# Optimization experiments

Hardware: AMD Instinct MI355X
Metric: run time of the kernel (lower is better)

The kernel has to match this reference:

```python
import jax, jax.numpy as jnp
import numpy as np

B, S, D = 64, 2048, 512

def setup_inputs() -> dict:
    key = jax.random.key(0)
    k1, k2, k3, k4, k5 = jax.random.split(key, 5)
    x = jax.random.normal(k1, (B, S, D), dtype=jnp.float32)
    # torch Linear(dim, dim): weight [D, D], bias [D]
    W1 = jax.random.normal(k2, (D, D), dtype=jnp.float32) * (1.0 / np.sqrt(D))
    b1 = jax.random.normal(k3, (D,), dtype=jnp.float32) * 0.01
    # torch Linear(dim, 1): weight [1, D] -> stored as [D], bias scalar
    w2 = jax.random.normal(k4, (D,), dtype=jnp.float32) * (1.0 / np.sqrt(D))
    b2 = jax.random.normal(k5, (), dtype=jnp.float32) * 0.01
    return {"x": x, "W1": W1, "b1": b1, "w2": w2, "b2": b2}

def reference(x, W1, b1, w2, b2):
    # score MLP: Linear -> Tanh -> Linear(->1), squeeze
    h = jnp.tanh(jnp.einsum('bsd,ed->bse', x, W1) + b1)   # [B,S,D]
    scores = jnp.einsum('bsd,d->bs', h, w2) + b2          # [B,S]
    w = jax.nn.softmax(scores, axis=1)[..., None]         # [B,S,1]
    ctx = jnp.sum(x * w, axis=1)                          # [B,D]
    return (ctx, w)
```

## Files before the change

### kernel.cpp

```cpp
#include <hip/hip_runtime.h>
#include <hip/hip_bf16.h>

#define BB 64
#define SS 2048
#define DD 512
#define MTOT (BB * SS)

typedef __attribute__((ext_vector_type(8))) short short8;
typedef __attribute__((ext_vector_type(4))) short s16x4;
typedef __attribute__((ext_vector_type(4))) float f32x4;

__device__ __forceinline__ short f2bf(float f){
  __hip_bfloat16 h = __float2bfloat16(f);
  return *reinterpret_cast<short*>(&h);
}
__device__ __forceinline__ short8 pack8(float4 a, float4 b){
  short8 u;
  u[0]=f2bf(a.x); u[1]=f2bf(a.y); u[2]=f2bf(a.z); u[3]=f2bf(a.w);
  u[4]=f2bf(b.x); u[5]=f2bf(b.y); u[6]=f2bf(b.z); u[7]=f2bf(b.w);
  return u;
}
__device__ __forceinline__ s16x4 pack4(float4 a){
  s16x4 u;
  u[0]=f2bf(a.x); u[1]=f2bf(a.y); u[2]=f2bf(a.z); u[3]=f2bf(a.w);
  return u;
}
__device__ __forceinline__ void gload_lds16(const unsigned short* g, unsigned short* l){
  __builtin_amdgcn_global_load_lds(
      (const __attribute__((address_space(1))) unsigned int*)g,
      (__attribute__((address_space(3))) unsigned int*)l, 16, 0, 0);
}

__global__ void cvt_w1_kernel(const float* __restrict__ W1, unsigned short* __restrict__ W1s){
  int i = blockIdx.x * blockDim.x + threadIdx.x;
  int s  = i >> 11;
  int g  = i & 2047;
  int kc = g >> 9;
  int e  = (g & 511) ^ kc;
  const float* src = W1 + (size_t)e * DD + s * 32 + kc * 8;
  float4 f0 = *(const float4*)src;
  float4 f1 = *(const float4*)(src + 4);
  *(short8*)(W1s + (size_t)i * 8) = pack8(f0, f1);
}

__launch_bounds__(512, 4)
__global__ void scores_kernel(const float* __restrict__ x,
                              const unsigned short* __restrict__ W1s,
                              const float* __restrict__ b1,
                              const float* __restrict__ w2,
                              float* __restrict__ scorep){
  __shared__ __align__(16) unsigned short Bbuf[2][16384];
  __shared__ __align__(16) unsigned short Abuf[2][2048];
  __shared__ float psum[8 * 64];

  const int t    = threadIdx.x;
  const int lane = t & 63;
  const int wid  = t >> 6;
  const int m0   = blockIdx.x * 64;
  const int arow = lane & 15;
  const int kgrp = lane >> 4;

  f32x4 acc[4][4];
  #pragma unroll
  for (int mt = 0; mt < 4; ++mt)
    #pragma unroll
    for (int et = 0; et < 4; ++et)
      acc[mt][et] = (f32x4){0.f, 0.f, 0.f, 0.f};

  const int ar = t >> 3;
  const int aq = t & 7;
  const float* asrc = x + (size_t)(m0 + ar) * DD + aq * 4;
  const int awoff = ((((ar << 2) + ((aq >> 1) ^ ((ar >> 1) & 3))) << 4) + ((aq & 1) << 3));

  const unsigned short* bsrc = W1s + ((size_t)((wid << 2) << 6) + lane) * 8;

  float4 areg[2];

  #pragma unroll
  for (int j = 0; j < 4; ++j)
    gload_lds16(bsrc + j * 512, &Bbuf[0][((wid << 2) + j) * 512]);
  float4 p0 = *(const float4*)asrc;
  areg[1] = *(const float4*)(asrc + 32);
  *(s16x4*)((char*)&Abuf[0][0] + awoff) = pack4(p0);
  asm volatile("s_waitcnt vmcnt(1)" ::: "memory");
  asm volatile("s_waitcnt lgkmcnt(0)" ::: "memory");
  __builtin_amdgcn_s_barrier();
  __builtin_amdgcn_sched_barrier(0);

  #pragma unroll
  for (int s = 0; s < 16; ++s){
    if (s < 15){
      const unsigned short* bs = bsrc + (size_t)(s + 1) * 16384;
      #pragma unroll
      for (int j = 0; j < 4; ++j)
        gload_lds16(bs + j * 512, &Bbuf[(s + 1) & 1][((wid << 2) + j) * 512]);
    }
    if (s < 14)
      areg[s & 1] = *(const float4*)(asrc + (s + 2) * 32);

    short8 af[4], bf[4];
    #pragma unroll
    for (int mt = 0; mt < 4; ++mt){
      int row = mt * 16 + arow;
      af[mt] = *(const short8*)((char*)&Abuf[s & 1][0]
                + (((row << 2) + (kgrp ^ ((row >> 1) & 3))) << 4));
    }
    #pragma unroll
    for (int et = 0; et < 4; ++et){
      int e = (wid << 6) + (et << 4) + arow;
      bf[et] = *(const short8*)((char*)&Bbuf[s & 1][0] + (((kgrp << 9) + (e ^ kgrp)) << 4));
    }

    __builtin_amdgcn_s_setprio(1);
    #pragma unroll
    for (int mt = 0; mt < 4; ++mt)
      #pragma unroll
      for (int et = 0; et < 4; ++et)
        acc[mt][et] = __builtin_amdgcn_mfma_f32_16x16x32_bf16(af[mt], bf[et], acc[mt][et], 0, 0, 0);
    __builtin_amdgcn_s_setprio(0);

    if (s < 15)
      *(s16x4*)((char*)&Abuf[(s + 1) & 1][0] + awoff) = pack4(areg[(s + 1) & 1]);

    if (s < 15){
      if (s < 14) asm volatile("s_waitcnt vmcnt(1)" ::: "memory");
      else        asm volatile("s_waitcnt vmcnt(0)" ::: "memory");
      asm volatile("s_waitcnt lgkmcnt(0)" ::: "memory");
      __builtin_amdgcn_s_barrier();
      __builtin_amdgcn_sched_barrier(0);
    }
  }

  float ps[4][4];
  #pragma unroll
  for (int mt = 0; mt < 4; ++mt)
    #pragma unroll
    for (int i = 0; i < 4; ++i) ps[mt][i] = 0.f;

  #pragma unroll
  for (int et = 0; et < 4; ++et){
    int e = (wid << 6) + (et << 4) + arow;
    float b1v = b1[e];
    float w2v = w2[e];
    #pragma unroll
    for (int mt = 0; mt < 4; ++mt){
      #pragma unroll
      for (int i = 0; i < 4; ++i){
        float g = acc[mt][et][i] + b1v;
        g = fminf(15.f, fmaxf(-15.f, g));
        float ex = __expf(2.f * g);
        ps[mt][i] += (1.f - 2.f / (ex + 1.f)) * w2v;
      }
    }
  }
  #pragma unroll
  for (int mt = 0; mt < 4; ++mt)
    #pragma unroll
    for (int i = 0; i < 4; ++i){
      float v = ps[mt][i];
      v += __shfl_xor(v, 1);
      v += __shfl_xor(v, 2);
      v += __shfl_xor(v, 4);
      v += __shfl_xor(v, 8);
      ps[mt][i] = v;
    }
  if ((lane & 15) == 0){
    #pragma unroll
    for (int mt = 0; mt < 4; ++mt)
      #pragma unroll
      for (int i = 0; i < 4; ++i)
        psum[wid * 64 + mt * 16 + (lane >> 4) * 4 + i] = ps[mt][i];
  }
  __syncthreads();
  if (t < 64){
    float ssum = 0.f;
    #pragma unroll
    for (int w = 0; w < 8; ++w) ssum += psum[w * 64 + t];
    scorep[m0 + t] = ssum;
  }
}

__global__ void softmax_kernel(const float* __restrict__ scorep, float* __restrict__ wout){
  const int b = blockIdx.x;
  const int t = threadIdx.x;
  float v[8];
  #pragma unroll
  for (int i = 0; i < 8; ++i) v[i] = scorep[(size_t)b * SS + t + i * 256];
  float m = v[0];
  #pragma unroll
  for (int i = 1; i < 8; ++i) m = fmaxf(m, v[i]);
  #pragma unroll
  for (int msk = 32; msk >= 1; msk >>= 1) m = fmaxf(m, __shfl_xor(m, msk));
  __shared__ float redm[4], reds[4];
  if ((t & 63) == 0) redm[t >> 6] = m;
  __syncthreads();
  m = fmaxf(fmaxf(redm[0], redm[1]), fmaxf(redm[2], redm[3]));
  float s = 0.f;
  #pragma unroll
  for (int i = 0; i < 8; ++i){ v[i] = __expf(v[i] - m); s += v[i]; }
  #pragma unroll
  for (int msk = 32; msk >= 1; msk >>= 1) s += __shfl_xor(s, msk);
  if ((t & 63) == 0) reds[t >> 6] = s;
  __syncthreads();
  s = reds[0] + reds[1] + reds[2] + reds[3];
  float inv = 1.f / s;
  #pragma unroll
  for (int i = 0; i < 8; ++i) wout[(size_t)b * SS + t + i * 256] = v[i] * inv;
}

__global__ void ctx_partial_kernel(const float* __restrict__ x, const float* __restrict__ wout,
                                   float* __restrict__ ctxp){
  __shared__ float red[4][512];
  const int t   = threadIdx.x;
  const int sub = t >> 7;
  const int dt  = t & 127;
  const int b   = blockIdx.x >> 3;
  const int sc  = blockIdx.x & 7;
  const float* xb = x + (size_t)b * SS * DD;
  const int s0 = sc * 256 + sub * 64;
  float4 acc = {0.f, 0.f, 0.f, 0.f};
  for (int s = s0; s < s0 + 64; ++s){
    float wv = wout[(size_t)b * SS + s];
    float4 xv = *(const float4*)(xb + (size_t)s * DD + dt * 4);
    acc.x += wv * xv.x; acc.y += wv * xv.y; acc.z += wv * xv.z; acc.w += wv * xv.w;
  }
  *(float4*)&red[sub][dt * 4] = acc;
  __syncthreads();
  if (t < 128){
    float4 r0 = *(const float4*)&red[0][t * 4];
    float4 r1 = *(const float4*)&red[1][t * 4];
    float4 r2 = *(const float4*)&red[2][t * 4];
    float4 r3 = *(const float4*)&red[3][t * 4];
    float4 o = { r0.x+r1.x+r2.x+r3.x, r0.y+r1.y+r2.y+r3.y,
                 r0.z+r1.z+r2.z+r3.z, r0.w+r1.w+r2.w+r3.w };
    *(float4*)&ctxp[((size_t)(b * 8 + sc)) * DD + t * 4] = o;
  }
}

__global__ void ctx_reduce_kernel(const float* __restrict__ ctxp, float* __restrict__ ctx){
  int i = blockIdx.x * blockDim.x + threadIdx.x;
  int b = i >> 9;
  int d = i & 511;
  float s = 0.f;
  #pragma unroll
  for (int sc = 0; sc < 8; ++sc) s += ctxp[((size_t)(b * 8 + sc)) * DD + d];
  ctx[(size_t)b * DD + d] = s;
}

extern "C" void kernel_launch(void* const* d_in, const int* in_sizes, int n_in,
                              void* d_out, int out_size, void* d_ws, size_t ws_size,
                              hipStream_t stream){
  const float* x  = (const float*)d_in[0];
  const float* W1 = (const float*)d_in[1];
  const float* b1 = (const float*)d_in[2];
  const float* w2 = (const float*)d_in[3];

  float* ctx  = (float*)d_out;
  float* wout = (float*)d_out + BB * DD;

  unsigned short* W1s = (unsigned short*)d_ws;
  float* scorep = (float*)((char*)d_ws + (512u << 10));
  float* ctxp   = (float*)d_ws;

  hipLaunchKernelGGL(cvt_w1_kernel,      dim3(128),  dim3(256), 0, stream, W1, W1s);
  hipLaunchKernelGGL(scores_kernel,      dim3(2048), dim3(512), 0, stream, x, W1s, b1, w2, scorep);
  hipLaunchKernelGGL(softmax_kernel,     dim3(64),   dim3(256), 0, stream, scorep, wout);
  hipLaunchKernelGGL(ctx_partial_kernel, dim3(512),  dim3(512), 0, stream, x, wout, ctxp);
  hipLaunchKernelGGL(ctx_reduce_kernel,  dim3(128),  dim3(256), 0, stream, ctxp, ctx);
}
```

Before: 169.2 us.

## Load W1 fragments directly into registers instead of staging through LDS

Removes the 64KB LDS double buffer for the bf16 W1 tile and the global_load_lds staging. Each wave now loads its MFMA B fragments straight from global (L2-resident) memory into registers, double-buffered across k-steps. The W1 conversion kernel becomes a plain row-major cast with no swizzle. This frees LDS for higher occupancy and cuts LDS reads, but relies on the compiler to insert the vmcnt waits and issues uncoalesced 16-byte global loads per lane.

Measured after the change: 220.6 us. 1.3x slower.

```diff
diff --git a/kernel.cpp b/kernel.cpp
--- a/kernel.cpp
+++ b/kernel.cpp
@@ -25,31 +25,21 @@
   u[0]=f2bf(a.x); u[1]=f2bf(a.y); u[2]=f2bf(a.z); u[3]=f2bf(a.w);
   return u;
 }
-__device__ __forceinline__ void gload_lds16(const unsigned short* g, unsigned short* l){
-  __builtin_amdgcn_global_load_lds(
-      (const __attribute__((address_space(1))) unsigned int*)g,
-      (__attribute__((address_space(3))) unsigned int*)l, 16, 0, 0);
-}
-
-__global__ void cvt_w1_kernel(const float* __restrict__ W1, unsigned short* __restrict__ W1s){
+
+__global__ void cvt_w1_kernel(const float* __restrict__ W1, unsigned short* __restrict__ W1b){
   int i = blockIdx.x * blockDim.x + threadIdx.x;
-  int s  = i >> 11;
-  int g  = i & 2047;
-  int kc = g >> 9;
-  int e  = (g & 511) ^ kc;
-  const float* src = W1 + (size_t)e * DD + s * 32 + kc * 8;
+  const float* src = W1 + (size_t)i * 8;
   float4 f0 = *(const float4*)src;
   float4 f1 = *(const float4*)(src + 4);
-  *(short8*)(W1s + (size_t)i * 8) = pack8(f0, f1);
+  *(short8*)(W1b + (size_t)i * 8) = pack8(f0, f1);
 }
 
 __launch_bounds__(512, 4)
 __global__ void scores_kernel(const float* __restrict__ x,
-                              const unsigned short* __restrict__ W1s,
+                              const unsigned short* __restrict__ W1b,
                               const float* __restrict__ b1,
                               const float* __restrict__ w2,
                               float* __restrict__ scorep){
-  __shared__ __align__(16) unsigned short Bbuf[2][16384];
   __shared__ __align__(16) unsigned short Abuf[2][2048];
   __shared__ float psum[8 * 64];
 
@@ -72,17 +62,22 @@
   const float* asrc = x + (size_t)(m0 + ar) * DD + aq * 4;
   const int awoff = ((((ar << 2) + ((aq >> 1) ^ ((ar >> 1) & 3))) << 4) + ((aq & 1) << 3));
 
-  const unsigned short* bsrc = W1s + ((size_t)((wid << 2) << 6) + lane) * 8;
-
+  const int e0 = (wid << 6) + arow;
+  const unsigned short* bp0 = W1b + (size_t)(e0 +  0) * DD + kgrp * 8;
+  const unsigned short* bp1 = W1b + (size_t)(e0 + 16) * DD + kgrp * 8;
+  const unsigned short* bp2 = W1b + (size_t)(e0 + 32) * DD + kgrp * 8;
+  const unsigned short* bp3 = W1b + (size_t)(e0 + 48) * DD + kgrp * 8;
+
+  short8 bb[2][4];
   float4 areg[2];
 
-  #pragma unroll
-  for (int j = 0; j < 4; ++j)
-    gload_lds16(bsrc + j * 512, &Bbuf[0][((wid << 2) + j) * 512]);
+  bb[0][0] = *(const short8*)bp0;
+  bb[0][1] = *(const short8*)bp1;
+  bb[0][2] = *(const short8*)bp2;
+  bb[0][3] = *(const short8*)bp3;
   float4 p0 = *(const float4*)asrc;
   areg[1] = *(const float4*)(asrc + 32);
   *(s16x4*)((char*)&Abuf[0][0] + awoff) = pack4(p0);
-  asm volatile("s_waitcnt vmcnt(1)" ::: "memory");
   asm volatile("s_waitcnt lgkmcnt(0)" ::: "memory");
   __builtin_amdgcn_s_barrier();
   __builtin_amdgcn_sched_barrier(0);
@@ -90,41 +85,30 @@
   #pragma unroll
   for (int s = 0; s < 16; ++s){
     if (s < 15){
-      const unsigned short* bs = bsrc + (size_t)(s + 1) * 16384;
-      #pragma unroll
-      for (int j = 0; j < 4; ++j)
-        gload_lds16(bs + j * 512, &Bbuf[(s + 1) & 1][((wid << 2) + j) * 512]);
+      bb[(s + 1) & 1][0] = *(const short8*)(bp0 + (s + 1) * 32);
+      bb[(s + 1) & 1][1] = *(const short8*)(bp1 + (s + 1) * 32);
+      bb[(s + 1) & 1][2] = *(const short8*)(bp2 + (s + 1) * 32);
+      bb[(s + 1) & 1][3] = *(const short8*)(bp3 + (s + 1) * 32);
     }
     if (s < 14)
       areg[s & 1] = *(const float4*)(asrc + (s + 2) * 32);
 
-    short8 af[4], bf[4];
+    __builtin_amdgcn_s_setprio(1);
     #pragma unroll
     for (int mt = 0; mt < 4; ++mt){
       int row = mt * 16 + arow;
-      af[mt] = *(const short8*)((char*)&Abuf[s & 1][0]
+      short8 af = *(const short8*)((char*)&Abuf[s & 1][0]
                 + (((row << 2) + (kgrp ^ ((row >> 1) & 3))) << 4));
-    }
-    #pragma unroll
-    for (int et = 0; et < 4; ++et){
-      int e = (wid << 6) + (et << 4) + arow;
-      bf[et] = *(const short8*)((char*)&Bbuf[s & 1][0] + (((kgrp << 9) + (e ^ kgrp)) << 4));
-    }
-
-    __builtin_amdgcn_s_setprio(1);
-    #pragma unroll
-    for (int mt = 0; mt < 4; ++mt)
       #pragma unroll
       for (int et = 0; et < 4; ++et)
-        acc[mt][et] = __builtin_amdgcn_mfma_f32_16x16x32_bf16(af[mt], bf[et], acc[mt][et], 0, 0, 0);
+        acc[mt][et] = __builtin_amdgcn_mfma_f32_16x16x32_bf16(af, bb[s & 1][et], acc[mt][et], 0, 0, 0);
+    }
     __builtin_amdgcn_s_setprio(0);
 
     if (s < 15)
       *(s16x4*)((char*)&Abuf[(s + 1) & 1][0] + awoff) = pack4(areg[(s + 1) & 1]);
 
     if (s < 15){
-      if (s < 14) asm volatile("s_waitcnt vmcnt(1)" ::: "memory");
-      else        asm volatile("s_waitcnt vmcnt(0)" ::: "memory");
       asm volatile("s_waitcnt lgkmcnt(0)" ::: "memory");
       __builtin_amdgcn_s_barrier();
       __builtin_amdgcn_sched_barrier(0);
@@ -258,12 +242,12 @@
   float* ctx  = (float*)d_out;
   float* wout = (float*)d_out + BB * DD;
 
-  unsigned short* W1s = (unsigned short*)d_ws;
+  unsigned short* W1b = (unsigned short*)d_ws;
   float* scorep = (float*)((char*)d_ws + (512u << 10));
   float* ctxp   = (float*)d_ws;
 
-  hipLaunchKernelGGL(cvt_w1_kernel,      dim3(128),  dim3(256), 0, stream, W1, W1s);
-  hipLaunchKernelGGL(scores_kernel,      dim3(2048), dim3(512), 0, stream, x, W1s, b1, w2, scorep);
+  hipLaunchKernelGGL(cvt_w1_kernel,      dim3(128),  dim3(256), 0, stream, W1, W1b);
+  hipLaunchKernelGGL(scores_kernel,      dim3(2048), dim3(512), 0, stream, x, W1b, b1, w2, scorep);
   hipLaunchKernelGGL(softmax_kernel,     dim3(64),   dim3(256), 0, stream, scorep, wout);
   hipLaunchKernelGGL(ctx_partial_kernel, dim3(512),  dim3(512), 0, stream, x, wout, ctxp);
   hipLaunchKernelGGL(ctx_reduce_kernel,  dim3(128),  dim3(256), 0, stream, ctxp, ctx);
```
